# Kernel optimization log

Measured on AMD Instinct MI355X. Metric: run time of the kernel, lower is better.

## Reference

```python
import jax, jax.numpy as jnp
import numpy as np

D_MODEL = 1024
D_INNER = 2 * D_MODEL        # mambapy default expand=2
D_STATE = 16                 # mambapy default
D_CONV = 4                   # mambapy default
DT_RANK = D_MODEL // 16      # ceil(1024/16) = 64
D_FF = 4 * D_MODEL
BATCH = 2
SEQ = 2048


def setup_inputs() -> dict:
    key = jax.random.key(0)
    ks = jax.random.split(key, 12)
    s = 0.02
    rn = lambda k, shape: jax.random.normal(k, shape, jnp.float32) * s
    inp = {
        'x': jax.random.normal(ks[0], (BATCH, SEQ, D_MODEL), jnp.float32),
        'ln1_w': jnp.ones((D_MODEL,), jnp.float32),
        'ln1_b': jnp.zeros((D_MODEL,), jnp.float32),
        'in_proj_w': rn(ks[1], (2 * D_INNER, D_MODEL)),
        'conv_w': rn(ks[2], (D_INNER, 1, D_CONV)),
        'conv_b': jnp.zeros((D_INNER,), jnp.float32),
        'x_proj_w': rn(ks[3], (DT_RANK + 2 * D_STATE, D_INNER)),
        'dt_w': rn(ks[4], (D_INNER, DT_RANK)),
        'dt_b': jax.random.normal(ks[5], (D_INNER,), jnp.float32) * 0.5 - 4.0,
        'A_log': jnp.log(jnp.broadcast_to(jnp.arange(1, D_STATE + 1, dtype=jnp.float32), (D_INNER, D_STATE))),
        'Dskip': jnp.ones((D_INNER,), jnp.float32),
        'out_proj_w': rn(ks[6], (D_MODEL, D_INNER)),
        'ln2_w': jnp.ones((D_MODEL,), jnp.float32),
        'ln2_b': jnp.zeros((D_MODEL,), jnp.float32),
        'ff1_w': rn(ks[7], (D_FF, D_MODEL)),
        'ff1_b': jnp.zeros((D_FF,), jnp.float32),
        'ff2_w': rn(ks[8], (D_MODEL, D_FF)),
        'ff2_b': jnp.zeros((D_MODEL,), jnp.float32),
    }
    return inp


def _layernorm(x, w, b, eps=1e-5):
    m = jnp.mean(x, -1, keepdims=True)
    v = jnp.var(x, -1, keepdims=True)
    return (x - m) * jax.lax.rsqrt(v + eps) * w + b


def _mamba(y, in_proj_w, conv_w, conv_b, x_proj_w, dt_w, dt_b, A_log, Dskip, out_proj_w):
    # y: [B, L, d_model]
    xz = y @ in_proj_w.T                       # [B, L, 2*d_inner]
    xc, z = jnp.split(xz, 2, axis=-1)
    # causal depthwise conv1d over seq
    xt = xc.transpose(0, 2, 1)                 # [B, d_inner, L]
    xt = jax.lax.conv_general_dilated(
        xt, conv_w, (1,), [(D_CONV - 1, 0)],
        dimension_numbers=('NCH', 'OIH', 'NCH'),
        feature_group_count=D_INNER) + conv_b[None, :, None]
    u = jax.nn.silu(xt.transpose(0, 2, 1))     # [B, L, d_inner]
    dbc = u @ x_proj_w.T                       # [B, L, dt_rank + 2*d_state]
    dlt = jax.nn.softplus(dbc[..., :DT_RANK] @ dt_w.T + dt_b)   # [B, L, d_inner]
    Bm = dbc[..., DT_RANK:DT_RANK + D_STATE]   # [B, L, d_state]
    Cm = dbc[..., DT_RANK + D_STATE:]          # [B, L, d_state]
    A = -jnp.exp(A_log)                        # [d_inner, d_state]

    def step(h, inp):
        d, Bt, Ct, ut = inp                    # [B,d_inner],[B,d_state],[B,d_state],[B,d_inner]
        h = jnp.exp(d[:, :, None] * A) * h + (d * ut)[:, :, None] * Bt[:, None, :]
        yt = jnp.einsum('bds,bs->bd', h, Ct)
        return h, yt

    h0 = jnp.zeros((y.shape[0], D_INNER, D_STATE), y.dtype)
    xs = (dlt.transpose(1, 0, 2), Bm.transpose(1, 0, 2), Cm.transpose(1, 0, 2), u.transpose(1, 0, 2))
    _, ys = jax.lax.scan(step, h0, xs)         # ys: [L, B, d_inner]
    ysc = ys.transpose(1, 0, 2) + u * Dskip
    return (ysc * jax.nn.silu(z)) @ out_proj_w.T


def reference(x, ln1_w, ln1_b, in_proj_w, conv_w, conv_b, x_proj_w, dt_w, dt_b,
              A_log, Dskip, out_proj_w, ln2_w, ln2_b, ff1_w, ff1_b, ff2_w, ff2_b):
    y = _layernorm(x, ln1_w, ln1_b)
    y = _mamba(y, in_proj_w, conv_w, conv_b, x_proj_w, dt_w, dt_b, A_log, Dskip, out_proj_w)
    y = _layernorm(y, ln2_w, ln2_b)
    h = jax.nn.gelu(y @ ff1_w.T + ff1_b, approximate=False)
    y = h @ ff2_w.T + ff2_b
    return x + y
```

## Files before the change

### kernel.cpp

```cpp
#include <hip/hip_runtime.h>

#define DEV __device__ __forceinline__

typedef float f32x4 __attribute__((ext_vector_type(4)));
typedef short bf16x8 __attribute__((ext_vector_type(8)));

DEV unsigned short f2bf(float f) {
  union { float f; unsigned int u; } v; v.f = f;
  unsigned int r = v.u + 0x7FFFu + ((v.u >> 16) & 1u);
  return (unsigned short)(r >> 16);
}
DEV float bf2f(unsigned short h) {
  union { unsigned int u; float f; } v; v.u = ((unsigned int)h) << 16;
  return v.f;
}

DEV float fexp2(float x) {
#if defined(__has_builtin)
#if __has_builtin(__builtin_amdgcn_exp2f)
  return __builtin_amdgcn_exp2f(x);
#else
  float r; asm("v_exp_f32 %0, %1" : "=v"(r) : "v"(x)); return r;
#endif
#else
  float r; asm("v_exp_f32 %0, %1" : "=v"(r) : "v"(x)); return r;
#endif
}

DEV void gload16(const void* g, void* l) {
  __builtin_amdgcn_global_load_lds((const __attribute__((address_space(1))) void*)g,
                                   (__attribute__((address_space(3))) void*)l, 16, 0, 0);
}

template <int BM, int BN, int EPI>
__global__ __launch_bounds__(256) void gemm_bt(
    const unsigned short* __restrict__ A, const unsigned short* __restrict__ B,
    float* __restrict__ O1, unsigned short* __restrict__ Ob, unsigned short* __restrict__ Ob2,
    const float* __restrict__ bias, const float* __restrict__ resid,
    int M, int N, int K, int Kstride)
{
  constexpr int MR = BM / 32, NR = BN / 32;
  __shared__ unsigned short As[BM * 64];
  __shared__ unsigned short Bs[BN * 64];
  const int tid = threadIdx.x;
  const int wave = tid >> 6;
  const int lane = tid & 63;
  const int brow = blockIdx.x * BM;
  const int bcol = blockIdx.y * BN;
  const int koff = blockIdx.z * K;
  const int wr = (wave >> 1) * (BM / 2), wc = (wave & 1) * (BN / 2);
  const int lr = lane & 15, lq = lane >> 4;

  f32x4 acc[MR][NR];
#pragma unroll
  for (int m = 0; m < MR; ++m)
#pragma unroll
    for (int n = 0; n < NR; ++n)
#pragma unroll
      for (int j = 0; j < 4; ++j) acc[m][n][j] = 0.f;

  const size_t strideA = (size_t)Kstride * 2;
  const char* Abase = (const char*)A + (size_t)brow * strideA + (size_t)koff * 2;
  const char* Bbase = (const char*)B + (size_t)bcol * strideA + (size_t)koff * 2;
  const int srow = tid >> 3;
  const int scol = (tid & 7) * 16;

  for (int k0 = 0; k0 < K; k0 += 64) {
#pragma unroll
    for (int is = 0; is < MR; ++is) {
      char* la = (char*)As + is * 4096 + wave * 1024;
      gload16(Abase + (size_t)(is * 32 + srow) * strideA + (size_t)k0 * 2 + scol, la);
    }
#pragma unroll
    for (int is = 0; is < NR; ++is) {
      char* lb = (char*)Bs + is * 4096 + wave * 1024;
      gload16(Bbase + (size_t)(is * 32 + srow) * strideA + (size_t)k0 * 2 + scol, lb);
    }
    asm volatile("s_waitcnt vmcnt(0)" ::: "memory");
    __syncthreads();
#pragma unroll
    for (int kk = 0; kk < 2; ++kk) {
      bf16x8 av[MR], bv[NR];
      const int ko = kk * 32 + lq * 8;
#pragma unroll
      for (int m = 0; m < MR; ++m)
        av[m] = *(const bf16x8*)&As[(wr + m * 16 + lr) * 64 + ko];
#pragma unroll
      for (int n = 0; n < NR; ++n)
        bv[n] = *(const bf16x8*)&Bs[(wc + n * 16 + lr) * 64 + ko];
#pragma unroll
      for (int m = 0; m < MR; ++m)
#pragma unroll
        for (int n = 0; n < NR; ++n)
          acc[m][n] = __builtin_amdgcn_mfma_f32_16x16x32_bf16(av[m], bv[n], acc[m][n], 0, 0, 0);
    }
    __syncthreads();
  }

#pragma unroll
  for (int m = 0; m < MR; ++m) {
#pragma unroll
    for (int n = 0; n < NR; ++n) {
      const int col = bcol + wc + n * 16 + lr;
      const int row0 = brow + wr + m * 16 + lq * 4;
#pragma unroll
      for (int j = 0; j < 4; ++j) {
        const int row = row0 + j;
        float v = acc[m][n][j];
        if (EPI == 0) {
          O1[(size_t)row * N + col] = v;
        } else if (EPI == 1) {
          v += bias[col];
          v = 0.5f * v * (1.f + erff(v * 0.70710678118654752f));
          Ob[(size_t)row * N + col] = f2bf(v);
        } else if (EPI == 2) {
          v += bias[col] + resid[(size_t)row * N + col];
          O1[(size_t)row * N + col] = v;
        } else if (EPI == 3) {
          v += bias[col];
          v = (v > 20.f) ? v : log1pf(expf(v));
          Ob[(size_t)row * N + col] = f2bf(v);
        } else if (EPI == 5) {
          if (col < 2048) Ob[(size_t)row * 2048 + col] = f2bf(v);
          else Ob2[(size_t)row * 2048 + (col - 2048)] = f2bf(v / (1.f + expf(-v)));
        } else {
          O1[((size_t)blockIdx.z * M + row) * N + col] = v;
        }
      }
    }
  }
}

__global__ __launch_bounds__(256) void xproj_reduce(
    const float* __restrict__ pbuf, float* __restrict__ dbc,
    unsigned short* __restrict__ adt)
{
  const int idx = blockIdx.x * 256 + threadIdx.x;
  float s = 0.f;
#pragma unroll
  for (int z = 0; z < 8; ++z) s += pbuf[(size_t)z * 524288 + idx];
  dbc[idx] = s;
  const int r = idx & 127;
  if (r < 64) adt[(size_t)(idx >> 7) * 64 + r] = f2bf(s);
}

__global__ __launch_bounds__(256) void ln_kernel(
    const float* __restrict__ x, const float* __restrict__ w,
    const float* __restrict__ b, unsigned short* __restrict__ out)
{
  const int row = blockIdx.x;
  const int tid = threadIdx.x;
  const float4 v = ((const float4*)(x + (size_t)row * 1024))[tid];
  float s = v.x + v.y + v.z + v.w;
  float sq = v.x * v.x + v.y * v.y + v.z * v.z + v.w * v.w;
#pragma unroll
  for (int m = 32; m >= 1; m >>= 1) { s += __shfl_xor(s, m); sq += __shfl_xor(sq, m); }
  __shared__ float ss[4], sqs[4];
  const int wave = tid >> 6;
  if ((tid & 63) == 0) { ss[wave] = s; sqs[wave] = sq; }
  __syncthreads();
  s = ss[0] + ss[1] + ss[2] + ss[3];
  sq = sqs[0] + sqs[1] + sqs[2] + sqs[3];
  const float mean = s * (1.f / 1024.f);
  const float var = sq * (1.f / 1024.f) - mean * mean;
  const float rstd = rsqrtf(var + 1e-5f);
  const float4 wv = ((const float4*)w)[tid];
  const float4 bv = ((const float4*)b)[tid];
  ushort4 o;
  o.x = f2bf((v.x - mean) * rstd * wv.x + bv.x);
  o.y = f2bf((v.y - mean) * rstd * wv.y + bv.y);
  o.z = f2bf((v.z - mean) * rstd * wv.z + bv.z);
  o.w = f2bf((v.w - mean) * rstd * wv.w + bv.w);
  ((ushort4*)(out + (size_t)row * 1024))[tid] = o;
}

__global__ __launch_bounds__(256) void conv_silu_kernel(
    const unsigned short* __restrict__ xc16, const float* __restrict__ cw,
    const float* __restrict__ cb, unsigned short* __restrict__ u16)
{
  const int idx = blockIdx.x * 256 + threadIdx.x;
  const int d = idx & 2047;
  const int i = idx >> 11;
  const int t = i & 2047;
  float acc = cb[d];
#pragma unroll
  for (int k = 0; k < 4; ++k) {
    const int tt = t - 3 + k;
    if (tt >= 0) acc += bf2f(xc16[(size_t)(i - 3 + k) * 2048 + d]) * cw[d * 4 + k];
  }
  const float s = acc / (1.f + expf(-acc));
  u16[idx] = f2bf(s);
}

__global__ __launch_bounds__(256) void cvt_weights(
    const float* __restrict__ w_in, unsigned short* __restrict__ d_in16,
    const float* __restrict__ w_ff1, unsigned short* __restrict__ d_ff1,
    const float* __restrict__ w_ff2, unsigned short* __restrict__ d_ff2,
    const float* __restrict__ w_out, unsigned short* __restrict__ d_out16,
    const float* __restrict__ w_dt, unsigned short* __restrict__ d_dt,
    const float* __restrict__ w_xp, unsigned short* __restrict__ d_xp)
{
  const int bid = blockIdx.x;
  const int tid = threadIdx.x;
  if (bid < 14336) {
    const float* s; unsigned short* d; int lb;
    if (bid < 4096)       { s = w_in;  d = d_in16;  lb = bid; }
    else if (bid < 8192)  { s = w_ff1; d = d_ff1;   lb = bid - 4096; }
    else if (bid < 12288) { s = w_ff2; d = d_ff2;   lb = bid - 8192; }
    else                  { s = w_out; d = d_out16; lb = bid - 12288; }
    const int i = lb * 256 + tid;
    const float4 v = ((const float4*)s)[i];
    ((ushort4*)d)[i] = make_ushort4(f2bf(v.x), f2bf(v.y), f2bf(v.z), f2bf(v.w));
  } else if (bid < 14464) {
    const int i = (bid - 14336) * 256 + tid;
    const float4 v = ((const float4*)w_dt)[i];
    ((ushort4*)d_dt)[i] = make_ushort4(f2bf(v.x), f2bf(v.y), f2bf(v.z), f2bf(v.w));
  } else {
    const int i = (bid - 14464) * 256 + tid;
    const int r = (i * 4) >> 11;
    ushort4 o;
    if (r < 96) {
      const float4 v = ((const float4*)w_xp)[i];
      o = make_ushort4(f2bf(v.x), f2bf(v.y), f2bf(v.z), f2bf(v.w));
    } else {
      o = make_ushort4(0, 0, 0, 0);
    }
    ((ushort4*)d_xp)[i] = o;
  }
}

template <int NC>
__global__ __launch_bounds__(256) void scan_p1(
    const unsigned short* __restrict__ dlt, const unsigned short* __restrict__ u16,
    const float* __restrict__ dbc, const float* __restrict__ A_log,
    float* __restrict__ hpart, float* __restrict__ sdtp)
{
  constexpr int L = 2048 / NC;
  const int tid = threadIdx.x;
  const int c = blockIdx.x % NC;
  const int chg = blockIdx.x / NC;
  const int id = chg * 256 + tid;
  const int dch = id & 2047;
  const int b = id >> 11;
  float al2[16], h[16];
#pragma unroll
  for (int s = 0; s < 16; ++s) {
    al2[s] = -fexp2(A_log[dch * 16 + s] * 1.44269504f) * 1.44269504f;
    h[s] = 0.f;
  }
  const int i0 = b * 2048 + c * L;
  const int i0u = __builtin_amdgcn_readfirstlane(i0);
  const unsigned short* dptr = dlt + (size_t)i0 * 2048 + dch;
  const unsigned short* uptr = u16 + (size_t)i0 * 2048 + dch;
  const float* Bptr = dbc + (size_t)i0u * 128 + 64;
  float sdt = 0.f;
  for (int t = 0; t < L; ++t) {
    const float dt = bf2f(*dptr);
    const float uu = bf2f(*uptr);
    const float dtu = dt * uu;
    const f32x4 B0 = *(const f32x4*)(Bptr + 0);
    const f32x4 B1 = *(const f32x4*)(Bptr + 4);
    const f32x4 B2 = *(const f32x4*)(Bptr + 8);
    const f32x4 B3 = *(const f32x4*)(Bptr + 12);
    sdt += dt;
#pragma unroll
    for (int s = 0; s < 16; ++s) {
      const float Bv = (s < 4) ? B0[s & 3] : (s < 8) ? B1[s & 3] : (s < 12) ? B2[s & 3] : B3[s & 3];
      h[s] = fexp2(dt * al2[s]) * h[s] + dtu * Bv;
    }
    dptr += 2048; uptr += 2048; Bptr += 128;
  }
  float* hp = hpart + ((size_t)(b * NC + c) * 2048 + dch) * 16;
#pragma unroll
  for (int s = 0; s < 16; ++s) hp[s] = h[s];
  sdtp[(size_t)(b * NC + c) * 2048 + dch] = sdt;
}

__global__ __launch_bounds__(256) void scan_prefix(
    const float* __restrict__ hpart, const float* __restrict__ sdtp,
    const float* __restrict__ A_log, float* __restrict__ hpre, int NC)
{
  const int g = blockIdx.x * 256 + threadIdx.x;
  const int s = g & 15;
  const int dch = (g >> 4) & 2047;
  const int b = g >> 15;
  const float al2 = -fexp2(A_log[dch * 16 + s] * 1.44269504f) * 1.44269504f;
  float run = 0.f;
  for (int c = 0; c < NC; ++c) {
    const size_t base = ((size_t)(b * NC + c) * 2048 + dch) * 16 + s;
    hpre[base] = run;
    run = fexp2(al2 * sdtp[(size_t)(b * NC + c) * 2048 + dch]) * run + hpart[base];
  }
}

template <int NC>
__global__ __launch_bounds__(256) void scan_p2(
    const unsigned short* __restrict__ dlt, const unsigned short* __restrict__ u16,
    const float* __restrict__ dbc, const unsigned short* __restrict__ zs16,
    const float* __restrict__ A_log, const float* __restrict__ Dskip,
    const float* __restrict__ hpre, unsigned short* __restrict__ gated)
{
  constexpr int L = 2048 / NC;
  const int tid = threadIdx.x;
  const int c = blockIdx.x % NC;
  const int chg = blockIdx.x / NC;
  const int id = chg * 256 + tid;
  const int dch = id & 2047;
  const int b = id >> 11;
  float al2[16], h[16];
#pragma unroll
  for (int s = 0; s < 16; ++s)
    al2[s] = -fexp2(A_log[dch * 16 + s] * 1.44269504f) * 1.44269504f;
  const float* hb = hpre + ((size_t)(b * NC + c) * 2048 + dch) * 16;
#pragma unroll
  for (int s = 0; s < 16; ++s) h[s] = hb[s];
  const float Dsk = Dskip[dch];
  const int i0 = b * 2048 + c * L;
  const int i0u = __builtin_amdgcn_readfirstlane(i0);
  const unsigned short* dptr = dlt + (size_t)i0 * 2048 + dch;
  const unsigned short* uptr = u16 + (size_t)i0 * 2048 + dch;
  const unsigned short* zptr = zs16 + (size_t)i0 * 2048 + dch;
  const float* Bptr = dbc + (size_t)i0u * 128 + 64;
  unsigned short* gptr = gated + (size_t)i0 * 2048 + dch;
  for (int t = 0; t < L; ++t) {
    const float dt = bf2f(*dptr);
    const float uu = bf2f(*uptr);
    const float zz = bf2f(*zptr);
    const float dtu = dt * uu;
    const f32x4 B0 = *(const f32x4*)(Bptr + 0);
    const f32x4 B1 = *(const f32x4*)(Bptr + 4);
    const f32x4 B2 = *(const f32x4*)(Bptr + 8);
    const f32x4 B3 = *(const f32x4*)(Bptr + 12);
    const f32x4 C0 = *(const f32x4*)(Bptr + 16);
    const f32x4 C1 = *(const f32x4*)(Bptr + 20);
    const f32x4 C2 = *(const f32x4*)(Bptr + 24);
    const f32x4 C3 = *(const f32x4*)(Bptr + 28);
    float y0 = 0.f, y1 = 0.f, y2 = 0.f, y3 = 0.f;
#pragma unroll
    for (int s = 0; s < 16; ++s) {
      const float Bv = (s < 4) ? B0[s & 3] : (s < 8) ? B1[s & 3] : (s < 12) ? B2[s & 3] : B3[s & 3];
      const float Cv = (s < 4) ? C0[s & 3] : (s < 8) ? C1[s & 3] : (s < 12) ? C2[s & 3] : C3[s & 3];
      h[s] = fexp2(dt * al2[s]) * h[s] + dtu * Bv;
      if ((s & 3) == 0) y0 += h[s] * Cv;
      else if ((s & 3) == 1) y1 += h[s] * Cv;
      else if ((s & 3) == 2) y2 += h[s] * Cv;
      else y3 += h[s] * Cv;
    }
    const float y = (y0 + y1) + (y2 + y3);
    *gptr = f2bf((y + uu * Dsk) * zz);
    dptr += 2048; uptr += 2048; zptr += 2048; Bptr += 128; gptr += 2048;
  }
}

extern "C" void kernel_launch(void* const* d_in, const int* in_sizes, int n_in,
                              void* d_out, int out_size, void* d_ws, size_t ws_size,
                              hipStream_t stream) {
  const float* x         = (const float*)d_in[0];
  const float* ln1_w     = (const float*)d_in[1];
  const float* ln1_b     = (const float*)d_in[2];
  const float* in_proj_w = (const float*)d_in[3];
  const float* conv_w    = (const float*)d_in[4];
  const float* conv_b    = (const float*)d_in[5];
  const float* x_proj_w  = (const float*)d_in[6];
  const float* dt_w      = (const float*)d_in[7];
  const float* dt_b      = (const float*)d_in[8];
  const float* A_log     = (const float*)d_in[9];
  const float* Dskip     = (const float*)d_in[10];
  const float* out_proj_w= (const float*)d_in[11];
  const float* ln2_w     = (const float*)d_in[12];
  const float* ln2_b     = (const float*)d_in[13];
  const float* ff1_w     = (const float*)d_in[14];
  const float* ff1_b     = (const float*)d_in[15];
  const float* ff2_w     = (const float*)d_in[16];
  const float* ff2_b     = (const float*)d_in[17];
  float* out = (float*)d_out;

  char* ws = (char*)d_ws;
  size_t off = 0;
  auto alloc = [&](size_t bytes) {
    char* p = ws + off;
    off += (bytes + 255) & ~(size_t)255;
    return p;
  };
  unsigned short* w16_in  = (unsigned short*)alloc(4096ull * 1024 * 2);
  unsigned short* w16_xp  = (unsigned short*)alloc(128ull * 2048 * 2);
  unsigned short* w16_dt  = (unsigned short*)alloc(2048ull * 64 * 2);
  unsigned short* w16_out = (unsigned short*)alloc(1024ull * 2048 * 2);
  unsigned short* w16_ff1 = (unsigned short*)alloc(4096ull * 1024 * 2);
  unsigned short* w16_ff2 = (unsigned short*)alloc(1024ull * 4096 * 2);
  unsigned short* y16     = (unsigned short*)alloc(4096ull * 1024 * 2);
  char* slotX             = alloc(4096ull * 2048 * 4);
  unsigned short* u16     = (unsigned short*)alloc(4096ull * 2048 * 2);
  char* slotA             = alloc(2048ull * 4096 * 4);
  unsigned short* zs16    = (unsigned short*)alloc(4096ull * 2048 * 2);
  float* dbc              = (float*)alloc(4096ull * 128 * 4);
  unsigned short* adt16   = (unsigned short*)alloc(4096ull * 64 * 2);
  char* slotD             = alloc(2048ull * 4096 * 4);
  (void)ws_size; (void)in_sizes; (void)n_in; (void)out_size;

  constexpr int NC = 128;
  unsigned short* xc16 = (unsigned short*)slotX;
  float* hpre  = (float*)slotX;
  float* c2 = (float*)slotX;
  unsigned short* t2_16 = (unsigned short*)(slotX + 4096ull * 1024 * 4);
  float* hpart = (float*)slotA;
  unsigned short* gated16 = (unsigned short*)slotA;
  unsigned short* h16 = (unsigned short*)slotA;
  float* pbuf  = (float*)slotD;
  unsigned short* dlt16 = (unsigned short*)slotD;
  float* sdtp  = (float*)y16;

  cvt_weights<<<14720, 256, 0, stream>>>(in_proj_w, w16_in, ff1_w, w16_ff1,
                                         ff2_w, w16_ff2, out_proj_w, w16_out,
                                         dt_w, w16_dt, x_proj_w, w16_xp);

  ln_kernel<<<4096, 256, 0, stream>>>(x, ln1_w, ln1_b, y16);
  gemm_bt<128, 128, 5><<<dim3(32, 32), 256, 0, stream>>>(y16, w16_in, nullptr, xc16, zs16, nullptr, nullptr, 4096, 4096, 1024, 1024);
  conv_silu_kernel<<<32768, 256, 0, stream>>>(xc16, conv_w, conv_b, u16);
  gemm_bt<128, 128, 6><<<dim3(32, 1, 8), 256, 0, stream>>>(u16, w16_xp, pbuf, nullptr, nullptr, nullptr, nullptr, 4096, 128, 256, 2048);
  xproj_reduce<<<2048, 256, 0, stream>>>(pbuf, dbc, adt16);
  gemm_bt<128, 128, 3><<<dim3(32, 16), 256, 0, stream>>>(adt16, w16_dt, nullptr, dlt16, nullptr, dt_b, nullptr, 4096, 2048, 64, 64);
  scan_p1<NC><<<16 * NC, 256, 0, stream>>>(dlt16, u16, dbc, A_log, hpart, sdtp);
  scan_prefix<<<256, 256, 0, stream>>>(hpart, sdtp, A_log, hpre, NC);
  scan_p2<NC><<<16 * NC, 256, 0, stream>>>(dlt16, u16, dbc, zs16, A_log, Dskip, hpre, gated16);
  gemm_bt<128, 64, 0><<<dim3(32, 16), 256, 0, stream>>>(gated16, w16_out, c2, nullptr, nullptr, nullptr, nullptr, 4096, 1024, 2048, 2048);
  ln_kernel<<<4096, 256, 0, stream>>>(c2, ln2_w, ln2_b, t2_16);
  gemm_bt<128, 128, 1><<<dim3(32, 32), 256, 0, stream>>>(t2_16, w16_ff1, nullptr, h16, nullptr, ff1_b, nullptr, 4096, 4096, 1024, 1024);
  gemm_bt<128, 64, 2><<<dim3(32, 16), 256, 0, stream>>>(h16, w16_ff2, out, nullptr, nullptr, ff2_b, x, 4096, 1024, 4096, 4096);
}
```

Before: 588.8 us.

## Split-K the out_proj and ff2 GEMMs, deepen x_proj split, narrow dt tiles

The out_proj and ff2 GEMMs now run as 2-way split-K into a partial buffer, followed by a new vectorized reduce kernel. For ff2 that reduce also adds the bias and residual, so the EPI==2 epilogue is removed. The x_proj split-K goes from 8 to 16 slices, and the dt GEMM uses 128x64 tiles to launch more blocks. The aim is to fill more CUs on GEMMs whose 512-block grids underuse the device, at the cost of extra partial-sum memory traffic and additional kernel launches.

Result: no change. 580.5 us (-1.4%).

```diff
diff --git a/kernel.cpp b/kernel.cpp
--- a/kernel.cpp
+++ b/kernel.cpp
@@ -113,9 +113,6 @@
           v += bias[col];
           v = 0.5f * v * (1.f + erff(v * 0.70710678118654752f));
           Ob[(size_t)row * N + col] = f2bf(v);
-        } else if (EPI == 2) {
-          v += bias[col] + resid[(size_t)row * N + col];
-          O1[(size_t)row * N + col] = v;
         } else if (EPI == 3) {
           v += bias[col];
           v = (v > 20.f) ? v : log1pf(expf(v));
@@ -131,6 +128,25 @@
   }
 }
 
+template <int FUSE>
+__global__ __launch_bounds__(256) void reduce2_kernel(
+    const float* __restrict__ pbuf, float* __restrict__ O1,
+    const float* __restrict__ bias, const float* __restrict__ resid)
+{
+  const int idx = blockIdx.x * 256 + threadIdx.x;
+  const float4 a = ((const float4*)pbuf)[idx];
+  const float4 b = ((const float4*)(pbuf + 4194304))[idx];
+  float4 o;
+  o.x = a.x + b.x; o.y = a.y + b.y; o.z = a.z + b.z; o.w = a.w + b.w;
+  if (FUSE == 1) {
+    const int col = (idx & 255) * 4;
+    const float4 bi = *(const float4*)(bias + col);
+    const float4 rv = ((const float4*)resid)[idx];
+    o.x += bi.x + rv.x; o.y += bi.y + rv.y; o.z += bi.z + rv.z; o.w += bi.w + rv.w;
+  }
+  ((float4*)O1)[idx] = o;
+}
+
 __global__ __launch_bounds__(256) void xproj_reduce(
     const float* __restrict__ pbuf, float* __restrict__ dbc,
     unsigned short* __restrict__ adt)
@@ -138,7 +154,7 @@
   const int idx = blockIdx.x * 256 + threadIdx.x;
   float s = 0.f;
 #pragma unroll
-  for (int z = 0; z < 8; ++z) s += pbuf[(size_t)z * 524288 + idx];
+  for (int z = 0; z < 16; ++z) s += pbuf[(size_t)z * 524288 + idx];
   dbc[idx] = s;
   const int r = idx & 127;
   if (r < 64) adt[(size_t)(idx >> 7) * 64 + r] = f2bf(s);
@@ -406,8 +422,9 @@
   float* hpart = (float*)slotA;
   unsigned short* gated16 = (unsigned short*)slotA;
   unsigned short* h16 = (unsigned short*)slotA;
-  float* pbuf  = (float*)slotD;
+  float* pbufX = (float*)slotD;
   unsigned short* dlt16 = (unsigned short*)slotD;
+  float* pbuf2 = (float*)slotD;
   float* sdtp  = (float*)y16;
 
   cvt_weights<<<14720, 256, 0, stream>>>(in_proj_w, w16_in, ff1_w, w16_ff1,
@@ -417,14 +434,16 @@
   ln_kernel<<<4096, 256, 0, stream>>>(x, ln1_w, ln1_b, y16);
   gemm_bt<128, 128, 5><<<dim3(32, 32), 256, 0, stream>>>(y16, w16_in, nullptr, xc16, zs16, nullptr, nullptr, 4096, 4096, 1024, 1024);
   conv_silu_kernel<<<32768, 256, 0, stream>>>(xc16, conv_w, conv_b, u16);
-  gemm_bt<128, 128, 6><<<dim3(32, 1, 8), 256, 0, stream>>>(u16, w16_xp, pbuf, nullptr, nullptr, nullptr, nullptr, 4096, 128, 256, 2048);
-  xproj_reduce<<<2048, 256, 0, stream>>>(pbuf, dbc, adt16);
-  gemm_bt<128, 128, 3><<<dim3(32, 16), 256, 0, stream>>>(adt16, w16_dt, nullptr, dlt16, nullptr, dt_b, nullptr, 4096, 2048, 64, 64);
+  gemm_bt<128, 128, 6><<<dim3(32, 1, 16), 256, 0, stream>>>(u16, w16_xp, pbufX, nullptr, nullptr, nullptr, nullptr, 4096, 128, 128, 2048);
+  xproj_reduce<<<2048, 256, 0, stream>>>(pbufX, dbc, adt16);
+  gemm_bt<128, 64, 3><<<dim3(32, 32), 256, 0, stream>>>(adt16, w16_dt, nullptr, dlt16, nullptr, dt_b, nullptr, 4096, 2048, 64, 64);
   scan_p1<NC><<<16 * NC, 256, 0, stream>>>(dlt16, u16, dbc, A_log, hpart, sdtp);
   scan_prefix<<<256, 256, 0, stream>>>(hpart, sdtp, A_log, hpre, NC);
   scan_p2<NC><<<16 * NC, 256, 0, stream>>>(dlt16, u16, dbc, zs16, A_log, Dskip, hpre, gated16);
-  gemm_bt<128, 64, 0><<<dim3(32, 16), 256, 0, stream>>>(gated16, w16_out, c2, nullptr, nullptr, nullptr, nullptr, 4096, 1024, 2048, 2048);
+  gemm_bt<128, 64, 6><<<dim3(32, 16, 2), 256, 0, stream>>>(gated16, w16_out, pbuf2, nullptr, nullptr, nullptr, nullptr, 4096, 1024, 1024, 2048);
+  reduce2_kernel<0><<<4096, 256, 0, stream>>>(pbuf2, c2, nullptr, nullptr);
   ln_kernel<<<4096, 256, 0, stream>>>(c2, ln2_w, ln2_b, t2_16);
   gemm_bt<128, 128, 1><<<dim3(32, 32), 256, 0, stream>>>(t2_16, w16_ff1, nullptr, h16, nullptr, ff1_b, nullptr, 4096, 4096, 1024, 1024);
-  gemm_bt<128, 64, 2><<<dim3(32, 16), 256, 0, stream>>>(h16, w16_ff2, out, nullptr, nullptr, ff2_b, x, 4096, 1024, 4096, 4096);
-}
+  gemm_bt<128, 64, 6><<<dim3(32, 16, 2), 256, 0, stream>>>(h16, w16_ff2, pbuf2, nullptr, nullptr, nullptr, nullptr, 4096, 1024, 2048, 4096);
+  reduce2_kernel<1><<<4096, 256, 0, stream>>>(pbuf2, out, ff2_b, x);
+}
```
